# Performance work log

Measured on AMD Instinct MI355X. Metric: run time of the kernel, lower is better.

## Reference

```python
import jax, jax.numpy as jnp
import numpy as np
import math

HEADS = 8
GROUPS = 4
PW = 2  # pooling_window
EPS = 1e-5


def group_norm(x, w, b, groups=GROUPS):
    # x: (B, C, *spatial); normalize over (C//groups, *spatial) per group
    B, C = x.shape[0], x.shape[1]
    xs = x.reshape(B, groups, -1)
    mu = xs.mean(-1, keepdims=True)
    var = xs.var(-1, keepdims=True)
    xs = (xs - mu) / jnp.sqrt(var + EPS)
    shape = (1, C) + (1,) * (x.ndim - 2)
    return xs.reshape(x.shape) * w.reshape(shape) + b.reshape(shape)


def cst_pool(x, pw=PW):
    # x: (B, C, Tq, Ts) with Ts = h*w + 1 (class token first); avg-pool spatial part
    cls_tok, sp = x[..., :1], x[..., 1:]
    B, C, Tq, S = sp.shape
    h = math.isqrt(S)
    sp = sp.reshape(B, C, Tq, h // pw, pw, h // pw, pw).mean(axis=(4, 6))
    return jnp.concatenate([cls_tok, sp.reshape(B, C, Tq, -1)], axis=-1)


def conv1x1(x, w):
    # w: (O, C); x: (B, C, Tq, Ts)
    return jnp.einsum('oc,bcqs->boqs', w, x)


def interp_bilinear_ac(m, n):
    # bilinear resize to (n, n), align_corners=True; m: (B, H, W) float
    def axis_interp(x, size, axis, L):
        c = jnp.linspace(0.0, L - 1.0, size)
        i0 = jnp.floor(c).astype(jnp.int32)
        i1 = jnp.minimum(i0 + 1, L - 1)
        f = (c - i0).astype(x.dtype)
        x0 = jnp.take(x, i0, axis=axis)
        x1 = jnp.take(x, i1, axis=axis)
        shape = [1] * x.ndim
        shape[axis] = size
        f = f.reshape(shape)
        return x0 * (1 - f) + x1 * f
    B, H, W = m.shape
    return axis_interp(axis_interp(m, n, 1, H), n, 2, W)


def setup_inputs() -> dict:
    key = jax.random.key(0)
    ks = jax.random.split(key, 8)
    B, Cin, Tq, Ts = 4, 128, 256, 257
    Cout = 512
    hidden = Cout // 2  # 256
    H = W = 256
    s = 0.05
    return {
        'corr_tokens': jax.random.normal(ks[0], (B, Cin, Tq, Ts), jnp.float32),
        's_masks': jax.random.randint(ks[1], (B, H, W), 0, 2, jnp.int32),
        'W_sc': jax.random.normal(ks[2], (Cout, Cin), jnp.float32) * s,
        'gn_sc_w': jnp.ones((Cout,), jnp.float32),
        'gn_sc_b': jnp.zeros((Cout,), jnp.float32),
        'W_qkv': jax.random.normal(ks[3], (3 * hidden, Cin), jnp.float32) * s,
        'b_qkv': jax.random.normal(ks[4], (3 * hidden,), jnp.float32) * s,
        'gn1_w': jnp.ones((hidden,), jnp.float32),
        'gn1_b': jnp.zeros((hidden,), jnp.float32),
        'W_agg': jax.random.normal(ks[5], (Cout, hidden), jnp.float32) * s,
        'gn2_w': jnp.ones((Cout,), jnp.float32),
        'gn2_b': jnp.zeros((Cout,), jnp.float32),
        'gn_out_w': jnp.ones((Cout,), jnp.float32),
        'gn_out_b': jnp.zeros((Cout,), jnp.float32),
    }


def reference(corr_tokens, s_masks, W_sc, gn_sc_w, gn_sc_b, W_qkv, b_qkv,
              gn1_w, gn1_b, W_agg, gn2_w, gn2_b, gn_out_w, gn_out_b):
    B, _, Tq, Ts = corr_tokens.shape
    hidden = W_qkv.shape[0] // 3
    E = hidden // HEADS

    # short_cut branch: conv1x1 -> CSTPooling -> GroupNorm -> ReLU
    residual = jax.nn.relu(group_norm(cst_pool(conv1x1(corr_tokens, W_sc)), gn_sc_w, gn_sc_b))

    # qkv projection
    qkv = conv1x1(corr_tokens, W_qkv) + b_qkv[None, :, None, None]
    qkv = qkv.reshape(B, 3, HEADS, E, Tq, Ts)  # channel order (x, g, e)
    q, k, v = qkv[:, 0], qkv[:, 1], qkv[:, 2]

    # pool queries over support-spatial dim: (B,G,E,Tq,Ts) -> (B,G,E,Tq,Td)
    q = cst_pool(q.reshape(B, hidden, Tq, Ts))
    Td = q.shape[-1]
    q = q.reshape(B, HEADS, E, Tq, Td)

    # per-query masked attention
    attn = jnp.einsum('bgeqd,bgeqs->bgqds', q, k)  # (B,G,Tq,Td,Ts)
    sdim = math.isqrt(Ts - 1)
    m = interp_bilinear_ac(jnp.minimum(s_masks, 1).astype(jnp.float32), sdim)
    m = m.reshape(B, 1, 1, 1, sdim * sdim)
    attn_seg = jnp.where(m == 0, jnp.float32(-1e9), attn[..., 1:])
    attn = jnp.concatenate([attn[..., :1], attn_seg], axis=-1)
    attn = jax.nn.softmax(attn, axis=-1)
    out = jnp.einsum('bgqds,bgeqs->bgeqd', attn, v).reshape(B, hidden, Tq, Td)

    # agg: GN -> ReLU -> conv1x1 -> GN -> ReLU
    out = jax.nn.relu(group_norm(out, gn1_w, gn1_b))
    out = conv1x1(out, W_agg)
    out = jax.nn.relu(group_norm(out, gn2_w, gn2_b))

    return group_norm(out + residual, gn_out_w, gn_out_b)
```

## Files before the change

kernel.cpp:

```cpp
#include <hip/hip_runtime.h>
#include <stdint.h>

#define NB    4
#define TQ    256
#define TS    257
#define TD    65
#define NPIX  16640
#define NPADQ 264
#define NPAD  67584
#define COUT  512
#define HID   256

typedef __attribute__((ext_vector_type(8))) short bf16x8;
typedef __attribute__((ext_vector_type(4))) float f32x4;

__device__ __forceinline__ float bf2f(unsigned short u) {
    union { unsigned int i; float f; } v; v.i = ((unsigned int)u) << 16; return v.f;
}
__device__ __forceinline__ unsigned short f2bf(float x) {
    union { float f; unsigned int i; } v; v.f = x;
    unsigned int r = v.i + 0x7fffu + ((v.i >> 16) & 1u);
    return (unsigned short)(r >> 16);
}

__device__ __forceinline__ float2 gn_params(const float* st, int bg, float invcnt) {
    float mu  = st[bg * 2] * invcnt;
    float var = st[bg * 2 + 1] * invcnt - mu * mu;
    float2 r; r.x = mu; r.y = rsqrtf(var + 1e-5f); return r;
}

__global__ void wprep_kernel(const float* __restrict__ wq, const float* __restrict__ wsc,
                             const float* __restrict__ wagg, unsigned short* __restrict__ wb) {
    int i = blockIdx.x * 256 + threadIdx.x;
    float v;
    if (i < 98304) v = wq[i];
    else if (i < 163840) v = wsc[i - 98304];
    else v = wagg[i - 163840];
    wb[i] = f2bf(v);
}

__global__ void mask_kernel(const int* __restrict__ sm, float* __restrict__ m16) {
    int b = blockIdx.x; int t = threadIdx.x;
    int i = t >> 4, j = t & 15;
    int v = sm[(size_t)b * 65536 + i * 17 * 256 + j * 17];
    m16[b * 256 + t] = (v != 0) ? 1.0f : 0.0f;
}

__global__ __launch_bounds__(256) void tpool_kernel(
    const float* __restrict__ corr,
    unsigned short* __restrict__ corrT,
    unsigned short* __restrict__ corrpT)
{
    int q = blockIdx.x, ch = blockIdx.y, b = blockIdx.z;
    int t = threadIdx.x;
    __shared__ unsigned short sT[264 * 66];

    {
        int laneT = t & 63; int crow = t >> 6;
        for (int c = crow; c < 64; c += 4) {
            const float* src = corr + (((size_t)b * 128 + ch * 64 + c) * 256 + q) * 257;
            for (int s = laneT; s < 257; s += 64) sT[s * 66 + c] = f2bf(src[s]);
        }
    }
    for (int idx = t; idx < 7 * 66; idx += 256) {
        int s = 257 + idx / 66, c = idx % 66;
        sT[s * 66 + c] = 0;
    }
    __syncthreads();

    {
        unsigned int* dst = (unsigned int*)corrT;
        size_t base = (size_t)b * (NPAD * 64) + (size_t)q * (264 * 64) + ch * 32;
        for (int idx = t; idx < 264 * 32; idx += 256) {
            int s = idx >> 5, cu = idx & 31;
            unsigned int v = (unsigned int)sT[s * 66 + 2 * cu] |
                             ((unsigned int)sT[s * 66 + 2 * cu + 1] << 16);
            dst[base + (size_t)s * 64 + cu] = v;
        }
    }
    {
        unsigned int* dst = (unsigned int*)corrpT;
        size_t base = (size_t)b * (NPIX * 64) + (size_t)q * (65 * 64) + ch * 32;
        for (int idx = t; idx < 65 * 32; idx += 256) {
            int d = idx >> 5, cu = idx & 31;
            float x0, x1;
            if (d == 0) {
                x0 = bf2f(sT[0 * 66 + 2 * cu]); x1 = bf2f(sT[0 * 66 + 2 * cu + 1]);
            } else {
                int dd = d - 1; int i = dd >> 3, j = dd & 7;
                int s = 1 + i * 32 + j * 2;
                int c0 = 2 * cu, c1 = 2 * cu + 1;
                x0 = 0.25f * (bf2f(sT[s*66+c0]) + bf2f(sT[(s+1)*66+c0]) +
                              bf2f(sT[(s+16)*66+c0]) + bf2f(sT[(s+17)*66+c0]));
                x1 = 0.25f * (bf2f(sT[s*66+c1]) + bf2f(sT[(s+1)*66+c1]) +
                              bf2f(sT[(s+16)*66+c1]) + bf2f(sT[(s+17)*66+c1]));
            }
            unsigned int v = (unsigned int)f2bf(x0) | ((unsigned int)f2bf(x1) << 16);
            dst[base + (size_t)d * 64 + cu] = v;
        }
    }
}

template<int MODE, int KT>
__global__ __launch_bounds__(256) void mgemm_kernel(
    const unsigned short* __restrict__ X,
    const unsigned short* __restrict__ Wb,
    int Nn,
    float* __restrict__ Yf,
    unsigned short* __restrict__ Y16,
    unsigned short* __restrict__ kb,
    unsigned short* __restrict__ vb,
    const float* __restrict__ bias,
    const float* __restrict__ st, const float* __restrict__ gw, const float* __restrict__ gb,
    float invcnt)
{
    int b  = blockIdx.z;
    int n0 = blockIdx.x * 128;
    int m0 = blockIdx.y * 128;
    int t = threadIdx.x;
    int w = t >> 6, lane = t & 63;
    int lm = lane & 15, lg = lane >> 4;
    int wn = (w & 1) * 64, wm = (w >> 1) * 64;

    __shared__ __align__(16) unsigned short sX[16384];
    __shared__ __align__(16) unsigned short sW[16384];

    f32x4 acc[4][4];
    #pragma unroll
    for (int i = 0; i < 4; i++)
        #pragma unroll
        for (int j = 0; j < 4; j++) { acc[i][j][0]=0.f; acc[i][j][1]=0.f; acc[i][j][2]=0.f; acc[i][j][3]=0.f; }

    for (int kc = 0; kc < KT / 128; kc++) {
        for (int i = t; i < 2048; i += 256) {
            int r_ = i >> 4, kq = i & 15;
            uint4 xv = *(const uint4*)&X[((size_t)b * Nn + n0 + r_) * KT + kc * 128 + (kq << 3)];
            if (MODE == 3) {
                union { uint4 v; unsigned short us[8]; } u; u.v = xv;
                int c0 = kc * 128 + (kq << 3);
                float2 p = gn_params(st, b * 4 + (c0 >> 6), invcnt);
                #pragma unroll
                for (int jj = 0; jj < 8; jj++) {
                    int cc = c0 + jj;
                    float v = bf2f(u.us[jj]);
                    v = fmaxf((v - p.x) * p.y * gw[cc] + gb[cc], 0.0f);
                    u.us[jj] = f2bf(v);
                }
                xv = u.v;
            }
            *(uint4*)&sX[r_ * 128 + ((kq ^ (r_ & 15)) << 3)] = xv;
            uint4 wv = *(const uint4*)&Wb[((size_t)(m0 + r_)) * KT + kc * 128 + (kq << 3)];
            *(uint4*)&sW[r_ * 128 + ((kq ^ (r_ & 15)) << 3)] = wv;
        }
        __syncthreads();
        #pragma unroll
        for (int kk = 0; kk < 4; kk++) {
            int kg = (kk << 2) | lg;
            bf16x8 af[4], bw[4];
            #pragma unroll
            for (int ii = 0; ii < 4; ii++)
                af[ii] = *(const bf16x8*)&sX[(wn + ii * 16 + lm) * 128 + ((kg ^ lm) << 3)];
            #pragma unroll
            for (int jj = 0; jj < 4; jj++)
                bw[jj] = *(const bf16x8*)&sW[(wm + jj * 16 + lm) * 128 + ((kg ^ lm) << 3)];
            #pragma unroll
            for (int ii = 0; ii < 4; ii++)
                #pragma unroll
                for (int jj = 0; jj < 4; jj++) {
                    if (MODE == 0)
                        acc[ii][jj] = __builtin_amdgcn_mfma_f32_16x16x32_bf16(bw[jj], af[ii], acc[ii][jj], 0,0,0);
                    else
                        acc[ii][jj] = __builtin_amdgcn_mfma_f32_16x16x32_bf16(af[ii], bw[jj], acc[ii][jj], 0,0,0);
                }
        }
        __syncthreads();
    }

    if (MODE == 0) {
        #pragma unroll
        for (int ii = 0; ii < 4; ii++) {
            int n = n0 + wn + ii * 16 + lm;
            #pragma unroll
            for (int jj = 0; jj < 4; jj++) {
                int mb = m0 + wm + jj * 16 + lg * 4;
                union { unsigned short us[4]; uint2 v; } pk;
                #pragma unroll
                for (int r = 0; r < 4; r++) pk.us[r] = f2bf(acc[ii][jj][r] + bias[mb + r]);
                *(uint2*)&Y16[((size_t)b * NPIX + n) * 256 + mb] = pk.v;
            }
        }
    } else if (MODE == 1) {
        if (m0 < 256) {
            #pragma unroll
            for (int ii = 0; ii < 4; ii++) {
                #pragma unroll
                for (int r = 0; r < 4; r++) {
                    unsigned int np = (unsigned int)(n0 + wn + ii * 16 + lg * 4 + r);
                    unsigned int qq = np / 264u;
                    unsigned int s  = np - qq * 264u;
                    #pragma unroll
                    for (int jj = 0; jj < 4; jj++) {
                        int m = m0 + wm + jj * 16 + lm;
                        int gch = m >> 5, e = m & 31;
                        kb[(((size_t)(b * 8 + gch) * 256 + qq) * 264 + s) * 32 + e] =
                            f2bf(acc[ii][jj][r] + bias[m]);
                    }
                }
            }
        } else {
            #pragma unroll
            for (int ii = 0; ii < 4; ii++) {
                int nb = n0 + wn + ii * 16 + lg * 4;
                #pragma unroll
                for (int jj = 0; jj < 4; jj++) {
                    int m = m0 + wm + jj * 16 + lm;
                    int mv = m - 256;
                    union { unsigned short us[4]; uint2 v; } pk;
                    #pragma unroll
                    for (int r = 0; r < 4; r++) pk.us[r] = f2bf(acc[ii][jj][r] + bias[m]);
                    *(uint2*)&vb[((size_t)b * 256 + mv) * NPAD + nb] = pk.v;
                }
            }
        }
    } else {
        #pragma unroll
        for (int ii = 0; ii < 4; ii++) {
            int nb = n0 + wn + ii * 16 + lg * 4;
            #pragma unroll
            for (int jj = 0; jj < 4; jj++) {
                int m = m0 + wm + jj * 16 + lm;
                *(f32x4*)&Yf[((size_t)b * COUT + m) * NPIX + nb] = acc[ii][jj];
            }
        }
    }
}

__global__ __launch_bounds__(320) void attn_kernel(
    const unsigned short* __restrict__ kb,
    const unsigned short* __restrict__ vb,
    const unsigned short* __restrict__ qpT,
    const float* __restrict__ m16,
    unsigned short* __restrict__ attT)
{
    int g = blockIdx.x, q = blockIdx.y, b = blockIdx.z;
    int t = threadIdx.x;
    int w = t >> 6, lane = t & 63;
    int lm = lane & 15, lg = lane >> 4;

    __shared__ __align__(16) unsigned short sP[23040];
    unsigned short* sPw = sP + w * 4608;

    int d = w * 16 + lm;
    int dc = d < 64 ? d : 64;
    bf16x8 qa = *(const bf16x8*)&qpT[((size_t)b * NPIX + q * 65 + dc) * 256 + g * 32 + lg * 8];
    if (d >= TD) { bf16x8 z = {}; qa = z; }

    f32x4 zero4 = {0.f, 0.f, 0.f, 0.f};
    f32x4 c[17];
    size_t kb0 = ((size_t)(b * 8 + g) * 256 + q) * (264 * 32);
    #pragma unroll
    for (int tt = 0; tt < 17; tt++) {
        bf16x8 kf = *(const bf16x8*)&kb[kb0 + (size_t)(tt * 16 + lm) * 32 + lg * 8];
        c[tt] = __builtin_amdgcn_mfma_f32_16x16x32_bf16(qa, kf, zero4, 0, 0, 0);
    }
    #pragma unroll
    for (int tt = 0; tt < 17; tt++) {
        int s = tt * 16 + lm;
        float mval = (s >= 1 && s < TS) ? m16[b * 256 + s - 1] : 0.0f;
        bool act = (s == 0) || (s < TS && mval != 0.0f);
        if (!act) { c[tt][0] = -1e9f; c[tt][1] = -1e9f; c[tt][2] = -1e9f; c[tt][3] = -1e9f; }
    }
    float inv[4];
    #pragma unroll
    for (int r = 0; r < 4; r++) {
        float mx = c[0][r];
        #pragma unroll
        for (int tt = 1; tt < 17; tt++) mx = fmaxf(mx, c[tt][r]);
        mx = fmaxf(mx, __shfl_xor(mx, 1)); mx = fmaxf(mx, __shfl_xor(mx, 2));
        mx = fmaxf(mx, __shfl_xor(mx, 4)); mx = fmaxf(mx, __shfl_xor(mx, 8));
        float sm = 0.f;
        #pragma unroll
        for (int tt = 0; tt < 17; tt++) { float e_ = __expf(c[tt][r] - mx); c[tt][r] = e_; sm += e_; }
        sm += __shfl_xor(sm, 1); sm += __shfl_xor(sm, 2);
        sm += __shfl_xor(sm, 4); sm += __shfl_xor(sm, 8);
        inv[r] = 1.0f / sm;
    }
    #pragma unroll
    for (int tt = 0; tt < 17; tt++) {
        int s = tt * 16 + lm;
        int sg = s >> 3, sl = s & 7;
        #pragma unroll
        for (int r = 0; r < 4; r++) {
            int dd = lg * 4 + r;
            sPw[dd * 288 + ((sg ^ (dd & 3)) << 3) + sl] = f2bf(c[tt][r] * inv[r]);
        }
    }
    for (int idx = lane; idx < 256; idx += 64) {
        int dd = idx >> 4, s = 272 + (idx & 15);
        int sg = s >> 3;
        sPw[dd * 288 + ((sg ^ (dd & 3)) << 3) + (s & 7)] = 0;
    }
    f32x4 o0 = zero4, o1 = zero4;
    size_t vb0 = ((size_t)b * 256 + g * 32) * NPAD + (size_t)q * 264;
    #pragma unroll
    for (int kk = 0; kk < 9; kk++) {
        int kg = kk * 4 + lg;
        bf16x8 pa = *(const bf16x8*)&sPw[lm * 288 + ((kg ^ (lm & 3)) << 3)];
        bf16x8 v0 = *(const bf16x8*)&vb[vb0 + (size_t)lm * NPAD + kk * 32 + lg * 8];
        bf16x8 v1 = *(const bf16x8*)&vb[vb0 + (size_t)(16 + lm) * NPAD + kk * 32 + lg * 8];
        o0 = __builtin_amdgcn_mfma_f32_16x16x32_bf16(pa, v0, o0, 0, 0, 0);
        o1 = __builtin_amdgcn_mfma_f32_16x16x32_bf16(pa, v1, o1, 0, 0, 0);
    }
    #pragma unroll
    for (int r = 0; r < 4; r++) {
        int dd = w * 16 + lg * 4 + r;
        if (dd < TD) {
            size_t nn = (size_t)b * NPIX + q * 65 + dd;
            attT[nn * 256 + g * 32 + lm]      = f2bf(o0[r]);
            attT[nn * 256 + g * 32 + 16 + lm] = f2bf(o1[r]);
        }
    }
}

__global__ void stats1_kernel(const unsigned short* __restrict__ attT, float* __restrict__ st) {
    int b = blockIdx.y;
    int t = threadIdx.x;
    int e8 = t & 31, g = e8 >> 3;
    int lane = t & 63;
    float s = 0.f, ss = 0.f;
    for (int r = blockIdx.x * 8 + (t >> 5); r < NPIX; r += gridDim.x * 8) {
        union { uint4 v; unsigned short us[8]; } u;
        u.v = *(const uint4*)&attT[((size_t)b * NPIX + r) * 256 + e8 * 8];
        #pragma unroll
        for (int j = 0; j < 8; j++) { float x = bf2f(u.us[j]); s += x; ss += x * x; }
    }
    s += __shfl_down(s, 32); ss += __shfl_down(ss, 32);
    s += __shfl_down(s, 4);  ss += __shfl_down(ss, 4);
    s += __shfl_down(s, 2);  ss += __shfl_down(ss, 2);
    s += __shfl_down(s, 1);  ss += __shfl_down(ss, 1);
    if (lane < 32 && (lane & 7) == 0) {
        atomicAdd(&st[(b * 4 + g) * 2],     s);
        atomicAdd(&st[(b * 4 + g) * 2 + 1], ss);
    }
}

__global__ void stats_kernel(const float* __restrict__ x, float* __restrict__ st, int Cg) {
    size_t len = (size_t)Cg * NPIX;
    size_t base = (size_t)blockIdx.y * len;
    const float4* x4 = reinterpret_cast<const float4*>(x + base);
    size_t len4 = len >> 2;
    float s = 0.f, ss = 0.f;
    for (size_t i = (size_t)blockIdx.x * blockDim.x + threadIdx.x; i < len4;
         i += (size_t)gridDim.x * blockDim.x) {
        float4 v = x4[i];
        s  += v.x + v.y + v.z + v.w;
        ss += v.x * v.x + v.y * v.y + v.z * v.z + v.w * v.w;
    }
    #pragma unroll
    for (int o = 32; o > 0; o >>= 1) { s += __shfl_down(s, o, 64); ss += __shfl_down(ss, o, 64); }
    __shared__ float red[4][2];
    int wid = threadIdx.x >> 6, lane = threadIdx.x & 63;
    if (lane == 0) { red[wid][0] = s; red[wid][1] = ss; }
    __syncthreads();
    if (threadIdx.x == 0) {
        float S  = red[0][0] + red[1][0] + red[2][0] + red[3][0];
        float SS = red[0][1] + red[1][1] + red[2][1] + red[3][1];
        atomicAdd(&st[blockIdx.y * 2],     S);
        atomicAdd(&st[blockIdx.y * 2 + 1], SS);
    }
}

__global__ void z_kernel(float* __restrict__ out, const float* __restrict__ scr,
                         const float* __restrict__ st2, const float* __restrict__ stsc,
                         const float* __restrict__ g2w, const float* __restrict__ g2b,
                         const float* __restrict__ gsw, const float* __restrict__ gsb)
{
    const float invcnt = 1.0f / (128.0f * NPIX);
    size_t total4 = (size_t)NB * COUT * (NPIX / 4);
    float4* o4 = reinterpret_cast<float4*>(out);
    const float4* s4 = reinterpret_cast<const float4*>(scr);
    for (size_t i = (size_t)blockIdx.x * blockDim.x + threadIdx.x; i < total4;
         i += (size_t)gridDim.x * blockDim.x) {
        size_t flat = i * 4;
        int c = (int)((flat / NPIX) % COUT);
        int b = (int)(flat / ((size_t)COUT * NPIX));
        int bg = b * 4 + (c >> 7);
        float2 p2 = gn_params(st2,  bg, invcnt);
        float2 ps = gn_params(stsc, bg, invcnt);
        float w2 = g2w[c] * p2.y, b2 = g2b[c] - p2.x * p2.y * g2w[c];
        float wsc = gsw[c] * ps.y, bsc = gsb[c] - ps.x * ps.y * gsw[c];
        float4 a = o4[i], r = s4[i], z;
        z.x = fmaxf(a.x * w2 + b2, 0.f) + fmaxf(r.x * wsc + bsc, 0.f);
        z.y = fmaxf(a.y * w2 + b2, 0.f) + fmaxf(r.y * wsc + bsc, 0.f);
        z.z = fmaxf(a.z * w2 + b2, 0.f) + fmaxf(r.z * wsc + bsc, 0.f);
        z.w = fmaxf(a.w * w2 + b2, 0.f) + fmaxf(r.w * wsc + bsc, 0.f);
        o4[i] = z;
    }
}

__global__ void norm_kernel(float* __restrict__ out, const float* __restrict__ st3,
                            const float* __restrict__ gw, const float* __restrict__ gb)
{
    const float invcnt = 1.0f / (128.0f * NPIX);
    size_t total4 = (size_t)NB * COUT * (NPIX / 4);
    float4* o4 = reinterpret_cast<float4*>(out);
    for (size_t i = (size_t)blockIdx.x * blockDim.x + threadIdx.x; i < total4;
         i += (size_t)gridDim.x * blockDim.x) {
        size_t flat = i * 4;
        int c = (int)((flat / NPIX) % COUT);
        int b = (int)(flat / ((size_t)COUT * NPIX));
        int bg = b * 4 + (c >> 7);
        float2 p = gn_params(st3, bg, invcnt);
        float w_ = gw[c] * p.y, b_ = gb[c] - p.x * p.y * gw[c];
        float4 a = o4[i], z;
        z.x = a.x * w_ + b_; z.y = a.y * w_ + b_; z.z = a.z * w_ + b_; z.w = a.w * w_ + b_;
        o4[i] = z;
    }
}

extern "C" void kernel_launch(void* const* d_in, const int* in_sizes, int n_in,
                              void* d_out, int out_size, void* d_ws, size_t ws_size,
                              hipStream_t stream) {
    (void)in_sizes; (void)n_in; (void)out_size; (void)ws_size;
    const float* corr     = (const float*)d_in[0];
    const int*   smask    = (const int*)  d_in[1];
    const float* W_sc     = (const float*)d_in[2];
    const float* gn_sc_w  = (const float*)d_in[3];
    const float* gn_sc_b  = (const float*)d_in[4];
    const float* W_qkv    = (const float*)d_in[5];
    const float* b_qkv    = (const float*)d_in[6];
    const float* gn1_w    = (const float*)d_in[7];
    const float* gn1_b    = (const float*)d_in[8];
    const float* W_agg    = (const float*)d_in[9];
    const float* gn2_w    = (const float*)d_in[10];
    const float* gn2_b    = (const float*)d_in[11];
    const float* gn_out_w = (const float*)d_in[12];
    const float* gn_out_b = (const float*)d_in[13];
    float* out = (float*)d_out;

    unsigned short* ws = (unsigned short*)d_ws;
    unsigned short* corrT  = ws;
    unsigned short* kbuf   = corrT  + (size_t)34603008;
    unsigned short* vbuf   = kbuf   + (size_t)69206016;
    unsigned short* corrpT = vbuf   + (size_t)69206016;
    unsigned short* qpT    = corrpT + (size_t)8519680;
    unsigned short* attT   = qpT    + (size_t)17047552;
    unsigned short* wbuf   = attT   + (size_t)17039360;
    float* m16   = (float*)(wbuf + (size_t)294912);
    float* stats = m16 + 1024;
    float* scr   = (float*)d_ws;
    float* st_sc = stats, *st1 = stats + 32, *st2 = stats + 64, *st3 = stats + 96;

    const float inv1 = 1.0f / (64.0f * (float)NPIX);

    hipMemsetAsync(stats, 0, 128 * sizeof(float), stream);
    wprep_kernel<<<dim3(1152), dim3(256), 0, stream>>>(W_qkv, W_sc, W_agg, wbuf);
    mask_kernel<<<dim3(NB), dim3(256), 0, stream>>>(smask, m16);
    tpool_kernel<<<dim3(TQ, 2, NB), dim3(256), 0, stream>>>(corr, corrT, corrpT);
    mgemm_kernel<0,128><<<dim3(130, 2, NB), dim3(256), 0, stream>>>(
        corrpT, wbuf, NPIX, nullptr, qpT, nullptr, nullptr, b_qkv,
        nullptr, nullptr, nullptr, 0.f);
    mgemm_kernel<1,128><<<dim3(528, 4, NB), dim3(256), 0, stream>>>(
        corrT, wbuf + 32768, NPAD, nullptr, nullptr, kbuf, vbuf, b_qkv + 256,
        nullptr, nullptr, nullptr, 0.f);
    attn_kernel<<<dim3(8, TQ, NB), dim3(320), 0, stream>>>(kbuf, vbuf, qpT, m16, attT);
    stats1_kernel<<<dim3(208, NB), dim3(256), 0, stream>>>(attT, st1);
    mgemm_kernel<3,256><<<dim3(130, 4, NB), dim3(256), 0, stream>>>(
        attT, wbuf + 163840, NPIX, out, nullptr, nullptr, nullptr, nullptr,
        st1, gn1_w, gn1_b, inv1);
    stats_kernel<<<dim3(64, 16), dim3(256), 0, stream>>>(out, st2, 128);
    mgemm_kernel<2,128><<<dim3(130, 4, NB), dim3(256), 0, stream>>>(
        corrpT, wbuf + 98304, NPIX, scr, nullptr, nullptr, nullptr, nullptr,
        nullptr, nullptr, nullptr, 0.f);
    stats_kernel<<<dim3(64, 16), dim3(256), 0, stream>>>(scr, st_sc, 128);
    z_kernel<<<dim3(4096), dim3(256), 0, stream>>>(out, scr, st2, st_sc, gn2_w, gn2_b, gn_sc_w, gn_sc_b);
    stats_kernel<<<dim3(64, 16), dim3(256), 0, stream>>>(out, st3, 128);
    norm_kernel<<<dim3(4096), dim3(256), 0, stream>>>(out, st3, gn_out_w, gn_out_b);
}
```

Before: 1.104 ms.

## Restructure attention kernel: swap MFMA operands, prefetch K/V, additive mask bias

```diff
diff --git a/kernel.cpp b/kernel.cpp
--- a/kernel.cpp
+++ b/kernel.cpp
@@ -39,11 +39,16 @@
     wb[i] = f2bf(v);
 }
 
-__global__ void mask_kernel(const int* __restrict__ sm, float* __restrict__ m16) {
+__global__ void mask_kernel(const int* __restrict__ sm, float* __restrict__ bias) {
     int b = blockIdx.x; int t = threadIdx.x;
-    int i = t >> 4, j = t & 15;
-    int v = sm[(size_t)b * 65536 + i * 17 * 256 + j * 17];
-    m16[b * 256 + t] = (v != 0) ? 1.0f : 0.0f;
+    if (t >= 272) return;
+    float v;
+    if (t == 0) v = 0.0f;
+    else if (t <= 256) {
+        int s = t - 1; int i = s >> 4, j = s & 15;
+        v = (sm[(size_t)b * 65536 + i * 17 * 256 + j * 17] != 0) ? 0.0f : -1e9f;
+    } else v = -1e9f;
+    bias[b * 272 + t] = v;
 }
 
 __global__ __launch_bounds__(256) void tpool_kernel(
@@ -235,11 +240,11 @@
     }
 }
 
-__global__ __launch_bounds__(320) void attn_kernel(
+__global__ __launch_bounds__(320, 3) void attn_kernel(
     const unsigned short* __restrict__ kb,
     const unsigned short* __restrict__ vb,
     const unsigned short* __restrict__ qpT,
-    const float* __restrict__ m16,
+    const float* __restrict__ bias272,
     unsigned short* __restrict__ attT)
 {
     int g = blockIdx.x, q = blockIdx.y, b = blockIdx.z;
@@ -255,61 +260,76 @@
     bf16x8 qa = *(const bf16x8*)&qpT[((size_t)b * NPIX + q * 65 + dc) * 256 + g * 32 + lg * 8];
     if (d >= TD) { bf16x8 z = {}; qa = z; }
 
+    size_t kb0 = ((size_t)(b * 8 + g) * 256 + q) * (264 * 32);
+    const unsigned short* kp = kb + kb0 + (size_t)lm * 32 + lg * 8;
+    bf16x8 kf[17];
+    #pragma unroll
+    for (int tt = 0; tt < 17; tt++)
+        kf[tt] = *(const bf16x8*)&kp[tt * 512];
+
     f32x4 zero4 = {0.f, 0.f, 0.f, 0.f};
     f32x4 c[17];
-    size_t kb0 = ((size_t)(b * 8 + g) * 256 + q) * (264 * 32);
+    #pragma unroll
+    for (int tt = 0; tt < 17; tt++)
+        c[tt] = __builtin_amdgcn_mfma_f32_16x16x32_bf16(kf[tt], qa, zero4, 0, 0, 0);
+
+    size_t vb0 = ((size_t)b * 256 + g * 32) * NPAD + (size_t)q * 264;
+    const unsigned short* vp = vb + vb0 + (size_t)lm * NPAD + lg * 8;
+    bf16x8 vf0[9], vf1[9];
+    #pragma unroll
+    for (int kk = 0; kk < 9; kk++) {
+        vf0[kk] = *(const bf16x8*)&vp[kk * 32];
+        vf1[kk] = *(const bf16x8*)&vp[16 * NPAD + kk * 32];
+    }
+
+    const float* bp = bias272 + b * 272 + lg * 4;
     #pragma unroll
     for (int tt = 0; tt < 17; tt++) {
-        bf16x8 kf = *(const bf16x8*)&kb[kb0 + (size_t)(tt * 16 + lm) * 32 + lg * 8];
-        c[tt] = __builtin_amdgcn_mfma_f32_16x16x32_bf16(qa, kf, zero4, 0, 0, 0);
-    }
+        f32x4 bf = *(const f32x4*)&bp[tt * 16];
+        c[tt][0] += bf[0]; c[tt][1] += bf[1]; c[tt][2] += bf[2]; c[tt][3] += bf[3];
+    }
+
+    f32x4 mv = c[0];
+    #pragma unroll
+    for (int tt = 1; tt < 17; tt++) {
+        mv[0] = fmaxf(mv[0], c[tt][0]); mv[1] = fmaxf(mv[1], c[tt][1]);
+        mv[2] = fmaxf(mv[2], c[tt][2]); mv[3] = fmaxf(mv[3], c[tt][3]);
+    }
+    float mx = fmaxf(fmaxf(mv[0], mv[1]), fmaxf(mv[2], mv[3]));
+    mx = fmaxf(mx, __shfl_xor(mx, 16));
+    mx = fmaxf(mx, __shfl_xor(mx, 32));
+    float sm = 0.f;
     #pragma unroll
     for (int tt = 0; tt < 17; tt++) {
-        int s = tt * 16 + lm;
-        float mval = (s >= 1 && s < TS) ? m16[b * 256 + s - 1] : 0.0f;
-        bool act = (s == 0) || (s < TS && mval != 0.0f);
-        if (!act) { c[tt][0] = -1e9f; c[tt][1] = -1e9f; c[tt][2] = -1e9f; c[tt][3] = -1e9f; }
-    }
-    float inv[4];
-    #pragma unroll
-    for (int r = 0; r < 4; r++) {
-        float mx = c[0][r];
-        #pragma unroll
-        for (int tt = 1; tt < 17; tt++) mx = fmaxf(mx, c[tt][r]);
-        mx = fmaxf(mx, __shfl_xor(mx, 1)); mx = fmaxf(mx, __shfl_xor(mx, 2));
-        mx = fmaxf(mx, __shfl_xor(mx, 4)); mx = fmaxf(mx, __shfl_xor(mx, 8));
-        float sm = 0.f;
-        #pragma unroll
-        for (int tt = 0; tt < 17; tt++) { float e_ = __expf(c[tt][r] - mx); c[tt][r] = e_; sm += e_; }
-        sm += __shfl_xor(sm, 1); sm += __shfl_xor(sm, 2);
-        sm += __shfl_xor(sm, 4); sm += __shfl_xor(sm, 8);
-        inv[r] = 1.0f / sm;
-    }
+        #pragma unroll
+        for (int r = 0; r < 4; r++) { float e_ = __expf(c[tt][r] - mx); c[tt][r] = e_; sm += e_; }
+    }
+    sm += __shfl_xor(sm, 16);
+    sm += __shfl_xor(sm, 32);
+    float inv = 1.0f / sm;
+
     #pragma unroll
     for (int tt = 0; tt < 17; tt++) {
-        int s = tt * 16 + lm;
-        int sg = s >> 3, sl = s & 7;
-        #pragma unroll
-        for (int r = 0; r < 4; r++) {
-            int dd = lg * 4 + r;
-            sPw[dd * 288 + ((sg ^ (dd & 3)) << 3) + sl] = f2bf(c[tt][r] * inv[r]);
-        }
-    }
-    for (int idx = lane; idx < 256; idx += 64) {
-        int dd = idx >> 4, s = 272 + (idx & 15);
-        int sg = s >> 3;
-        sPw[dd * 288 + ((sg ^ (dd & 3)) << 3) + (s & 7)] = 0;
-    }
+        union { unsigned short us[4]; uint2 v; } pk;
+        #pragma unroll
+        for (int r = 0; r < 4; r++) pk.us[r] = f2bf(c[tt][r] * inv);
+        int sg = tt * 2 + (lg >> 1);
+        int off = lm * 288 + ((sg ^ (lm & 3)) << 3) + (lg & 1) * 4;
+        *(uint2*)&sPw[off] = pk.v;
+    }
+    if (lg < 2) {
+        int sg = 34 + lg;
+        uint4 z4 = {0u, 0u, 0u, 0u};
+        *(uint4*)&sPw[lm * 288 + ((sg ^ (lm & 3)) << 3)] = z4;
+    }
+
     f32x4 o0 = zero4, o1 = zero4;
-    size_t vb0 = ((size_t)b * 256 + g * 32) * NPAD + (size_t)q * 264;
     #pragma unroll
     for (int kk = 0; kk < 9; kk++) {
         int kg = kk * 4 + lg;
         bf16x8 pa = *(const bf16x8*)&sPw[lm * 288 + ((kg ^ (lm & 3)) << 3)];
-        bf16x8 v0 = *(const bf16x8*)&vb[vb0 + (size_t)lm * NPAD + kk * 32 + lg * 8];
-        bf16x8 v1 = *(const bf16x8*)&vb[vb0 + (size_t)(16 + lm) * NPAD + kk * 32 + lg * 8];
-        o0 = __builtin_amdgcn_mfma_f32_16x16x32_bf16(pa, v0, o0, 0, 0, 0);
-        o1 = __builtin_amdgcn_mfma_f32_16x16x32_bf16(pa, v1, o1, 0, 0, 0);
+        o0 = __builtin_amdgcn_mfma_f32_16x16x32_bf16(pa, vf0[kk], o0, 0, 0, 0);
+        o1 = __builtin_amdgcn_mfma_f32_16x16x32_bf16(pa, vf1[kk], o1, 0, 0, 0);
     }
     #pragma unroll
     for (int r = 0; r < 4; r++) {
@@ -444,10 +464,10 @@
     unsigned short* vbuf   = kbuf   + (size_t)69206016;
     unsigned short* corrpT = vbuf   + (size_t)69206016;
     unsigned short* qpT    = corrpT + (size_t)8519680;
-    unsigned short* attT   = qpT    + (size_t)17047552;
+    unsigned short* attT   = qpT    + (size_t)17039360;
     unsigned short* wbuf   = attT   + (size_t)17039360;
-    float* m16   = (float*)(wbuf + (size_t)294912);
-    float* stats = m16 + 1024;
+    float* bias  = (float*)(wbuf + (size_t)294912);
+    float* stats = bias + 1088;
     float* scr   = (float*)d_ws;
     float* st_sc = stats, *st1 = stats + 32, *st2 = stats + 64, *st3 = stats + 96;
 
@@ -455,7 +475,7 @@
 
     hipMemsetAsync(stats, 0, 128 * sizeof(float), stream);
     wprep_kernel<<<dim3(1152), dim3(256), 0, stream>>>(W_qkv, W_sc, W_agg, wbuf);
-    mask_kernel<<<dim3(NB), dim3(256), 0, stream>>>(smask, m16);
+    mask_kernel<<<dim3(NB), dim3(320), 0, stream>>>(smask, bias);
     tpool_kernel<<<dim3(TQ, 2, NB), dim3(256), 0, stream>>>(corr, corrT, corrpT);
     mgemm_kernel<0,128><<<dim3(130, 2, NB), dim3(256), 0, stream>>>(
         corrpT, wbuf, NPIX, nullptr, qpT, nullptr, nullptr, b_qkv,
@@ -463,7 +483,7 @@
     mgemm_kernel<1,128><<<dim3(528, 4, NB), dim3(256), 0, stream>>>(
         corrT, wbuf + 32768, NPAD, nullptr, nullptr, kbuf, vbuf, b_qkv + 256,
         nullptr, nullptr, nullptr, 0.f);
-    attn_kernel<<<dim3(8, TQ, NB), dim3(320), 0, stream>>>(kbuf, vbuf, qpT, m16, attT);
+    attn_kernel<<<dim3(8, TQ, NB), dim3(320), 0, stream>>>(kbuf, vbuf, qpT, bias, attT);
     stats1_kernel<<<dim3(208, NB), dim3(256), 0, stream>>>(attT, st1);
     mgemm_kernel<3,256><<<dim3(130, 4, NB), dim3(256), 0, stream>>>(
         attT, wbuf + 163840, NPIX, out, nullptr, nullptr, nullptr, nullptr,
```

Measured after the change: 1.059 ms. -4.1%, faster.
